# Kernel optimization log

Hardware: AMD Instinct MI355X
Metric: run time of the kernel (lower is better)

## Reference

```python
import jax, jax.numpy as jnp
import numpy as np

INV_DELTA = 15.0  # init kwarg inv_delta
EPS = 1e-12       # torch F.normalize eps


def setup_inputs() -> dict:
    key = jax.random.key(0)
    k1, k2 = jax.random.split(key)
    features = jax.random.normal(k1, (32, 256, 30, 30), dtype=jnp.float32)
    # _embedding buffer: randn clamped to >= 0
    embedding = jnp.maximum(jax.random.normal(k2, (2048, 256), dtype=jnp.float32), 0.0)
    # _min_distance_mean buffer, initialized to 0.5
    min_distance_mean = jnp.ones((1,), dtype=jnp.float32) * 0.5
    return {"features": features, "embedding": embedding,
            "min_distance_mean": min_distance_mean}


def reference(features, embedding, min_distance_mean):
    # crop 1-pixel border: [B,C,H,W] -> [B,C,H-2,W-2]
    f = features[:, :, 1:-1, 1:-1]
    # squared euclidean distance to each codeword via GEMM trick:
    # dist[b,k,h,w] = ||f[b,:,h,w]||^2 + ||e[k]||^2 - 2 <f, e[k]>
    f2 = jnp.sum(f * f, axis=1, keepdims=True)                 # [B,1,H',W']
    e2 = jnp.sum(embedding * embedding, axis=1)                # [K]
    xe = jnp.einsum('bchw,kc->bkhw', f, embedding)             # 1x1-conv GEMM
    dist = f2 + e2[None, :, None, None] - 2.0 * xe             # [B,K,H',W']
    # adaptive temperature softmax over codewords
    inv_delta_adaptive = INV_DELTA / min_distance_mean[0]
    codes = jax.nn.softmax(-inv_delta_adaptive * dist, axis=1)  # [B,K,H',W']
    # global average pool + L1 normalize
    bow = jnp.mean(codes, axis=(2, 3))                          # [B,K]
    bow = bow / jnp.maximum(jnp.sum(jnp.abs(bow), axis=1, keepdims=True), EPS)
    return (bow, codes)
```

## Files before the change

kernel.cpp:

```cpp
#include <hip/hip_runtime.h>
#include <hip/hip_bf16.h>
#include <math.h>

typedef __attribute__((ext_vector_type(8))) short bf16x8;
typedef __attribute__((ext_vector_type(16))) float f32x16;

#define B_ 32
#define C_ 256
#define K_ 2048
#define HW_ 784
#define NPIX 25088
#define FEAT_BSTRIDE 230400
#define FEAT_CSTRIDE 900
#define INV_DELTA 15.0f
#define LOG2E 1.4426950408889634f
#define QSCALE 409.6f
#define QDEC (LOG2E / QSCALE)

#define BM 128
#define BN 128
#define BKC 32
#define NCH 8
#define NSLAB 16

#define AS1 __attribute__((address_space(1)))
#define AS3 __attribute__((address_space(3)))

__device__ __forceinline__ ushort f2bf(float x) {
    __hip_bfloat16 h = __float2bfloat16(x);
    return *reinterpret_cast<ushort*>(&h);
}
__device__ __forceinline__ float bf2f(ushort u) {
    __hip_bfloat16 h;
    *reinterpret_cast<ushort*>(&h) = u;
    return __bfloat162float(h);
}
__device__ __forceinline__ void gl_lds16(const ushort* g, ushort* l) {
    __builtin_amdgcn_global_load_lds((AS1 const uint*)g, (AS3 uint*)l, 16, 0, 0);
}

__global__ void e2_kernel(const float* __restrict__ emb, float* __restrict__ e2) {
    int t = threadIdx.x;
    int wid = t >> 6, lane = t & 63;
    int k = blockIdx.x * 4 + wid;
    const float* er = emb + (size_t)k * C_;
    float v0 = er[lane], v1 = er[lane + 64], v2 = er[lane + 128], v3 = er[lane + 192];
    float s = v0 * v0 + v1 * v1 + v2 * v2 + v3 * v3;
#pragma unroll
    for (int off = 32; off > 0; off >>= 1) s += __shfl_xor(s, off);
    if (lane == 0) e2[k] = s;
}

__global__ void prep_e_kernel(const float* __restrict__ emb,
                              ushort* __restrict__ ehi, ushort* __restrict__ elo) {
    int i = blockIdx.x * 256 + threadIdx.x;
    float v = emb[i];
    ushort h = f2bf(v);
    float r = v - bf2f(h);
    ehi[i] = h;
    elo[i] = f2bf(r);
}

__global__ __launch_bounds__(256) void prep_f_kernel(const float* __restrict__ feat,
                                                     ushort* __restrict__ fhi,
                                                     ushort* __restrict__ flo) {
    __shared__ float F[256 * 65];
    int t = threadIdx.x;
    int px0 = blockIdx.x * 64;
    {
        int lane = t & 63, cq = t >> 6;
        int px = px0 + lane;
        int b = px / HW_, hw = px % HW_;
        int h = hw / 28, w = hw % 28;
        const float* base = feat + (size_t)b * FEAT_BSTRIDE + (size_t)(h + 1) * 30 + (w + 1);
#pragma unroll
        for (int cc = 0; cc < 64; ++cc) {
            int c = cq * 64 + cc;
            F[c * 65 + lane] = base[(size_t)c * FEAT_CSTRIDE];
        }
    }
    __syncthreads();
    {
        int px_l = t >> 2, cseg = t & 3;
        size_t ob = (size_t)(px0 + px_l) * C_ + cseg * 64;
        uint uh[32], ul[32];
#pragma unroll
        for (int j = 0; j < 32; ++j) {
            float v0 = F[(cseg * 64 + 2 * j) * 65 + px_l];
            float v1 = F[(cseg * 64 + 2 * j + 1) * 65 + px_l];
            ushort h0 = f2bf(v0), h1 = f2bf(v1);
            float r0 = v0 - bf2f(h0), r1 = v1 - bf2f(h1);
            uh[j] = (uint)h0 | ((uint)h1 << 16);
            ul[j] = (uint)f2bf(r0) | ((uint)f2bf(r1) << 16);
        }
#pragma unroll
        for (int j = 0; j < 8; ++j) {
            *reinterpret_cast<uint4*>(&fhi[ob + j * 8]) = *reinterpret_cast<uint4*>(&uh[j * 4]);
            *reinterpret_cast<uint4*>(&flo[ob + j * 8]) = *reinterpret_cast<uint4*>(&ul[j * 4]);
        }
    }
}

__global__ __launch_bounds__(256, 3) void gemm_kernel(
    const ushort* __restrict__ fhi, const ushort* __restrict__ flo,
    const ushort* __restrict__ ehi, const ushort* __restrict__ elo,
    const float* __restrict__ mdm, const float* __restrict__ e2g,
    ushort* __restrict__ zq, float* __restrict__ m_part, float* __restrict__ l_part)
{
    __shared__ __align__(16) ushort Asmem[2][2][BM * BKC];
    __shared__ float redA[2][132];
    __shared__ float redM[132];
    uint* zT = reinterpret_cast<uint*>(Asmem);

    int t = threadIdx.x;
    int lane = t & 63, wid = t >> 6;
    int wrow = wid >> 1, wcol = wid & 1;
    int g = lane >> 5, ci = lane & 31;

    int bid = blockIdx.x;
    int swz = (bid & 7) * 392 + (bid >> 3);
    int tile = swz >> 4, slab = swz & 15;
    int px0 = tile * BM;
    int k0 = slab * BN;

    auto stageA = [&](int buf, int ch) {
        int c0 = ch * BKC;
#pragma unroll
        for (int i = 0; i < 2; ++i) {
            int p = t + i * 256;
            int rp = p >> 3, q = p & 7;
            int v = q ^ (rp & 7);
            int row = rp * 2 + (v >> 2);
            int cu = (v & 3) * 8;
            size_t ga = (size_t)(px0 + row) * C_ + c0 + cu;
            gl_lds16(fhi + ga, &Asmem[buf][0][p * 8]);
            gl_lds16(flo + ga, &Asmem[buf][1][p * 8]);
        }
    };

    const ushort* pbh[2];
    const ushort* pbl[2];
#pragma unroll
    for (int ni = 0; ni < 2; ++ni) {
        size_t r = (size_t)(k0 + wcol * 64 + ni * 32 + ci) * C_ + g * 8;
        pbh[ni] = ehi + r;
        pbl[ni] = elo + r;
    }
    bf16x8 bhS[2][2], bvS[2][2];
    auto loadB = [&](int slot, int gs) {
        int off = gs * 16;
#pragma unroll
        for (int ni = 0; ni < 2; ++ni) {
            bhS[slot][ni] = *reinterpret_cast<const bf16x8*>(pbh[ni] + off);
            bvS[slot][ni] = *reinterpret_cast<const bf16x8*>(pbl[ni] + off);
        }
    };

    f32x16 acc[2][2];
#pragma unroll
    for (int mi = 0; mi < 2; ++mi)
#pragma unroll
        for (int ni = 0; ni < 2; ++ni)
            acc[mi][ni] = (f32x16)(0.0f);

    int xr = (ci >> 1) & 7;
    int bb4 = (ci & 1) * 4;
    int rpA0 = wrow * 32 + (ci >> 1);

    stageA(0, 0);
    loadB(0, 0);
    asm volatile("s_waitcnt vmcnt(4)" ::: "memory");
    __builtin_amdgcn_s_barrier();

#pragma unroll
    for (int ch = 0; ch < NCH; ++ch) {
        if (ch + 1 < NCH) stageA((ch + 1) & 1, ch + 1);
#pragma unroll
        for (int s = 0; s < 2; ++s) {
            int gs = ch * 2 + s;
            if (gs + 1 < 2 * NCH) loadB((gs + 1) & 1, gs + 1);
            __builtin_amdgcn_sched_barrier(0);
            int qs = (bb4 + s * 2 + g) ^ xr;
            bf16x8 ah[2], av[2];
#pragma unroll
            for (int mi = 0; mi < 2; ++mi) {
                int off = (rpA0 + mi * 16) * 64 + qs * 8;
                ah[mi] = *reinterpret_cast<const bf16x8*>(&Asmem[ch & 1][0][off]);
                av[mi] = *reinterpret_cast<const bf16x8*>(&Asmem[ch & 1][1][off]);
            }
            int cs = gs & 1;
#pragma unroll
            for (int mi = 0; mi < 2; ++mi)
#pragma unroll
                for (int ni = 0; ni < 2; ++ni) {
                    acc[mi][ni] = __builtin_amdgcn_mfma_f32_32x32x16_bf16(ah[mi], bhS[cs][ni], acc[mi][ni], 0, 0, 0);
                    acc[mi][ni] = __builtin_amdgcn_mfma_f32_32x32x16_bf16(ah[mi], bvS[cs][ni], acc[mi][ni], 0, 0, 0);
                    acc[mi][ni] = __builtin_amdgcn_mfma_f32_32x32x16_bf16(av[mi], bhS[cs][ni], acc[mi][ni], 0, 0, 0);
                }
        }
        if (ch + 1 < NCH) {
            asm volatile("s_waitcnt vmcnt(4)" ::: "memory");
            __builtin_amdgcn_s_barrier();
        }
    }

    const float alpha = INV_DELTA / mdm[0];
    float e2v[2];
#pragma unroll
    for (int ni = 0; ni < 2; ++ni) e2v[ni] = e2g[k0 + wcol * 64 + ni * 32 + ci];
#pragma unroll
    for (int mi = 0; mi < 2; ++mi)
#pragma unroll
        for (int ni = 0; ni < 2; ++ni)
            acc[mi][ni] = alpha * (2.0f * acc[mi][ni] - e2v[ni]);

    float ms[2][16];
    {
        float mt[2][16];
#pragma unroll
        for (int mi = 0; mi < 2; ++mi)
#pragma unroll
            for (int r = 0; r < 16; ++r)
                mt[mi][r] = fmaxf(acc[mi][0][r], acc[mi][1][r]);
#pragma unroll
        for (int off = 1; off < 32; off <<= 1)
#pragma unroll
            for (int mi = 0; mi < 2; ++mi)
#pragma unroll
                for (int r = 0; r < 16; ++r)
                    mt[mi][r] = fmaxf(mt[mi][r], __shfl_xor(mt[mi][r], off));
        if (ci == 0) {
#pragma unroll
            for (int mi = 0; mi < 2; ++mi)
#pragma unroll
                for (int r = 0; r < 16; ++r)
                    redA[wcol][wrow * 64 + mi * 32 + (r & 3) + 8 * (r >> 2) + 4 * g] = mt[mi][r];
        }
    }
    __syncthreads();
    if (t < 128) redM[t] = fmaxf(redA[0][t], redA[1][t]);
    __syncthreads();
#pragma unroll
    for (int mi = 0; mi < 2; ++mi)
#pragma unroll
        for (int r = 0; r < 16; ++r)
            ms[mi][r] = redM[wrow * 64 + mi * 32 + (r & 3) + 8 * (r >> 2) + 4 * g];

    {
        float lt[2][16];
#pragma unroll
        for (int mi = 0; mi < 2; ++mi)
#pragma unroll
            for (int r = 0; r < 16; ++r)
                lt[mi][r] = exp2f((acc[mi][0][r] - ms[mi][r]) * LOG2E) +
                            exp2f((acc[mi][1][r] - ms[mi][r]) * LOG2E);
#pragma unroll
        for (int off = 1; off < 32; off <<= 1)
#pragma unroll
            for (int mi = 0; mi < 2; ++mi)
#pragma unroll
                for (int r = 0; r < 16; ++r)
                    lt[mi][r] += __shfl_xor(lt[mi][r], off);
        if (ci == 0) {
#pragma unroll
            for (int mi = 0; mi < 2; ++mi)
#pragma unroll
                for (int r = 0; r < 16; ++r)
                    redA[wcol][wrow * 64 + mi * 32 + (r & 3) + 8 * (r >> 2) + 4 * g] = lt[mi][r];
        }
    }
    __syncthreads();
    if (t < 128) {
        m_part[(size_t)slab * NPIX + px0 + t] = redM[t];
        l_part[(size_t)slab * NPIX + px0 + t] = redA[0][t] + redA[1][t];
    }

#pragma unroll
    for (int mi = 0; mi < 2; ++mi)
#pragma unroll
        for (int ni = 0; ni < 2; ++ni) {
            int kl = wcol * 64 + ni * 32 + ci;
#pragma unroll
            for (int r = 0; r < 16; r += 2) {
                int row = wrow * 64 + mi * 32 + (r & 3) + 8 * (r >> 2) + 4 * g;
                float s0 = fmaxf((acc[mi][ni][r]     - ms[mi][r])     * QSCALE, -32760.f);
                float s1 = fmaxf((acc[mi][ni][r + 1] - ms[mi][r + 1]) * QSCALE, -32760.f);
                int q0 = (int)s0, q1 = (int)s1;
                uint u = ((uint)(ushort)(short)q0) | (((uint)(ushort)(short)q1) << 16);
                int pp = row >> 1;
                int seg = pp >> 2;
                zT[kl * 64 + ((seg ^ (kl & 15)) << 2) + (pp & 3)] = u;
            }
        }
    __syncthreads();

    const uint4* zT4 = reinterpret_cast<const uint4*>(zT);
#pragma unroll
    for (int it = 0; it < 8; ++it) {
        int kl = (t >> 4) + it * 16;
        int seg = t & 15;
        uint4 v = zT4[kl * 16 + (seg ^ (kl & 15))];
        int k = k0 + kl;
        int pxx = px0 + seg * 8;
        int bb = pxx / HW_, hh = pxx - bb * HW_;
        *reinterpret_cast<uint4*>(&zq[((size_t)bb * K_ + k) * HW_ + hh]) = v;
    }
}

__global__ void combine_kernel(const float* __restrict__ m_part, const float* __restrict__ l_part,
                               float* __restrict__ m_fin, float* __restrict__ rl_g) {
    int p = blockIdx.x * 256 + threadIdx.x;
    float m = -3.4e38f;
#pragma unroll
    for (int s = 0; s < NSLAB; ++s) m = fmaxf(m, m_part[(size_t)s * NPIX + p]);
    float l = 0.f;
#pragma unroll
    for (int s = 0; s < NSLAB; ++s)
        l += l_part[(size_t)s * NPIX + p] * exp2f((m_part[(size_t)s * NPIX + p] - m) * LOG2E);
    m_fin[p] = m;
    rl_g[p] = 1.0f / l;
}

__global__ __launch_bounds__(256) void finish_kernel(
    const ushort* __restrict__ zq, const float* __restrict__ m_part,
    const float* __restrict__ m_fin, const float* __restrict__ rl_g,
    float* __restrict__ codes, float* __restrict__ bow)
{
    __shared__ float corr[HW_], rls[HW_];
    __shared__ float bsum[64][4];
    int t = threadIdx.x;
    int kc = blockIdx.x, b = blockIdx.y;
    int slab = kc >> 1;
    for (int i = t; i < HW_; i += 256) {
        int p = b * HW_ + i;
        corr[i] = (m_part[(size_t)slab * NPIX + p] - m_fin[p]) * LOG2E;
        rls[i] = rl_g[p];
    }
    __syncthreads();
    int wid = t >> 6, lane = t & 63;
    for (int kl = 0; kl < 64; ++kl) {
        int k = kc * 64 + kl;
        size_t base = ((size_t)b * K_ + k) * HW_;
        float ssum = 0.f;
        if (t < 196) {
            uint2 raw = *reinterpret_cast<const uint2*>(&zq[base + t * 4]);
            int q0 = (int)(short)(raw.x & 0xffffu), q1 = (int)(short)(raw.x >> 16);
            int q2 = (int)(short)(raw.y & 0xffffu), q3 = (int)(short)(raw.y >> 16);
            float4 out;
            out.x = exp2f(fmaf((float)q0, QDEC, corr[t * 4 + 0])) * rls[t * 4 + 0];
            out.y = exp2f(fmaf((float)q1, QDEC, corr[t * 4 + 1])) * rls[t * 4 + 1];
            out.z = exp2f(fmaf((float)q2, QDEC, corr[t * 4 + 2])) * rls[t * 4 + 2];
            out.w = exp2f(fmaf((float)q3, QDEC, corr[t * 4 + 3])) * rls[t * 4 + 3];
            *reinterpret_cast<float4*>(&codes[base + t * 4]) = out;
            ssum = out.x + out.y + out.z + out.w;
        }
#pragma unroll
        for (int off = 32; off > 0; off >>= 1) ssum += __shfl_xor(ssum, off);
        if (lane == 0) bsum[kl][wid] = ssum;
    }
    __syncthreads();
    if (t < 64) {
        float s = bsum[t][0] + bsum[t][1] + bsum[t][2] + bsum[t][3];
        bow[(size_t)b * K_ + kc * 64 + t] = s * (1.0f / 784.0f);
    }
}

__global__ void bownorm_kernel(float* __restrict__ bow) {
    __shared__ float wred[4];
    __shared__ float denom_s;
    int b = blockIdx.x, t = threadIdx.x;
    float* row = bow + (size_t)b * K_;
    float v[8];
    float s = 0.f;
#pragma unroll
    for (int i = 0; i < 8; ++i) {
        v[i] = row[t + i * 256];
        s += fabsf(v[i]);
    }
#pragma unroll
    for (int off = 32; off > 0; off >>= 1) s += __shfl_xor(s, off);
    int wid = t >> 6, lane = t & 63;
    if (lane == 0) wred[wid] = s;
    __syncthreads();
    if (t == 0) denom_s = fmaxf(wred[0] + wred[1] + wred[2] + wred[3], 1e-12f);
    __syncthreads();
    float denom = denom_s;
#pragma unroll
    for (int i = 0; i < 8; ++i) row[t + i * 256] = v[i] / denom;
}

extern "C" void kernel_launch(void* const* d_in, const int* in_sizes, int n_in,
                              void* d_out, int out_size, void* d_ws, size_t ws_size,
                              hipStream_t stream) {
    const float* feat = (const float*)d_in[0];
    const float* emb  = (const float*)d_in[1];
    const float* mdm  = (const float*)d_in[2];
    float* bow   = (float*)d_out;
    float* codes = bow + (size_t)B_ * K_;

    char* ws = (char*)d_ws;
    size_t off = 0;
    auto alloc = [&](size_t bytes) { char* p = ws + off; off = (off + bytes + 255) & ~(size_t)255; return p; };
    ushort* ehi    = (ushort*)alloc((size_t)K_ * C_ * 2);
    ushort* elo    = (ushort*)alloc((size_t)K_ * C_ * 2);
    float*  e2     = (float*)alloc(K_ * 4);
    float*  m_part = (float*)alloc((size_t)NSLAB * NPIX * 4);
    float*  l_part = (float*)alloc((size_t)NSLAB * NPIX * 4);
    float*  m_fin  = (float*)alloc((size_t)NPIX * 4);
    float*  rl_g   = (float*)alloc((size_t)NPIX * 4);
    ushort* zq     = (ushort*)alloc((size_t)NPIX * K_ * 2);

    ushort* fhi = (ushort*)codes;
    ushort* flo = fhi + (size_t)NPIX * C_;

    e2_kernel<<<512, 256, 0, stream>>>(emb, e2);
    prep_e_kernel<<<2048, 256, 0, stream>>>(emb, ehi, elo);
    prep_f_kernel<<<392, 256, 0, stream>>>(feat, fhi, flo);
    gemm_kernel<<<3136, 256, 0, stream>>>(fhi, flo, ehi, elo, mdm, e2, zq, m_part, l_part);
    combine_kernel<<<98, 256, 0, stream>>>(m_part, l_part, m_fin, rl_g);
    finish_kernel<<<dim3(32, 32), 256, 0, stream>>>(zq, m_part, m_fin, rl_g, codes, bow);
    bownorm_kernel<<<32, 256, 0, stream>>>(bow);
}
```

Baseline: 233.4 us.

## Swap MFMA operands so accumulators hold per-pixel columns and store directly

The MFMA operand order is swapped so each lane's accumulator fragment covers codewords for a single pixel. The per-pixel max and sum-exp reductions then need one cross-lane shuffle instead of a five-step butterfly. The LDS transpose staging and its extra barrier before the quantized output store are removed, and each lane now writes 2-byte values straight to global memory. The risk is less efficient global writes: each row becomes a 64-byte segment of 2-byte stores instead of 16-byte vector stores, on a very large output tensor.

```diff
diff --git a/kernel.cpp b/kernel.cpp
--- a/kernel.cpp
+++ b/kernel.cpp
@@ -107,10 +107,9 @@
     const float* __restrict__ mdm, const float* __restrict__ e2g,
     ushort* __restrict__ zq, float* __restrict__ m_part, float* __restrict__ l_part)
 {
-    __shared__ __align__(16) ushort Asmem[2][2][BM * BKC];
+    __shared__ __align__(16) ushort Fsmem[2][2][BM * BKC];
     __shared__ float redA[2][132];
     __shared__ float redM[132];
-    uint* zT = reinterpret_cast<uint*>(Asmem);
 
     int t = threadIdx.x;
     int lane = t & 63, wid = t >> 6;
@@ -123,7 +122,7 @@
     int px0 = tile * BM;
     int k0 = slab * BN;
 
-    auto stageA = [&](int buf, int ch) {
+    auto stageF = [&](int buf, int ch) {
         int c0 = ch * BKC;
 #pragma unroll
         for (int i = 0; i < 2; ++i) {
@@ -133,26 +132,26 @@
             int row = rp * 2 + (v >> 2);
             int cu = (v & 3) * 8;
             size_t ga = (size_t)(px0 + row) * C_ + c0 + cu;
-            gl_lds16(fhi + ga, &Asmem[buf][0][p * 8]);
-            gl_lds16(flo + ga, &Asmem[buf][1][p * 8]);
+            gl_lds16(fhi + ga, &Fsmem[buf][0][p * 8]);
+            gl_lds16(flo + ga, &Fsmem[buf][1][p * 8]);
         }
     };
 
-    const ushort* pbh[2];
-    const ushort* pbl[2];
+    const ushort* peh[2];
+    const ushort* pel[2];
 #pragma unroll
     for (int ni = 0; ni < 2; ++ni) {
         size_t r = (size_t)(k0 + wcol * 64 + ni * 32 + ci) * C_ + g * 8;
-        pbh[ni] = ehi + r;
-        pbl[ni] = elo + r;
-    }
-    bf16x8 bhS[2][2], bvS[2][2];
-    auto loadB = [&](int slot, int gs) {
+        peh[ni] = ehi + r;
+        pel[ni] = elo + r;
+    }
+    bf16x8 ehS[2][2], elS[2][2];
+    auto loadE = [&](int slot, int gs) {
         int off = gs * 16;
 #pragma unroll
         for (int ni = 0; ni < 2; ++ni) {
-            bhS[slot][ni] = *reinterpret_cast<const bf16x8*>(pbh[ni] + off);
-            bvS[slot][ni] = *reinterpret_cast<const bf16x8*>(pbl[ni] + off);
+            ehS[slot][ni] = *reinterpret_cast<const bf16x8*>(peh[ni] + off);
+            elS[slot][ni] = *reinterpret_cast<const bf16x8*>(pel[ni] + off);
         }
     };
 
@@ -165,37 +164,37 @@
 
     int xr = (ci >> 1) & 7;
     int bb4 = (ci & 1) * 4;
-    int rpA0 = wrow * 32 + (ci >> 1);
-
-    stageA(0, 0);
-    loadB(0, 0);
-    asm volatile("s_waitcnt vmcnt(4)" ::: "memory");
+    int rpF0 = wrow * 32 + (ci >> 1);
+
+    stageF(0, 0);
+    loadE(0, 0);
+    asm volatile("s_waitcnt vmcnt(2)" ::: "memory");
     __builtin_amdgcn_s_barrier();
 
 #pragma unroll
     for (int ch = 0; ch < NCH; ++ch) {
-        if (ch + 1 < NCH) stageA((ch + 1) & 1, ch + 1);
+        if (ch + 1 < NCH) stageF((ch + 1) & 1, ch + 1);
 #pragma unroll
         for (int s = 0; s < 2; ++s) {
             int gs = ch * 2 + s;
-            if (gs + 1 < 2 * NCH) loadB((gs + 1) & 1, gs + 1);
+            if (gs + 1 < 2 * NCH) loadE((gs + 1) & 1, gs + 1);
             __builtin_amdgcn_sched_barrier(0);
             int qs = (bb4 + s * 2 + g) ^ xr;
-            bf16x8 ah[2], av[2];
+            bf16x8 fh[2], fl[2];
 #pragma unroll
             for (int mi = 0; mi < 2; ++mi) {
-                int off = (rpA0 + mi * 16) * 64 + qs * 8;
-                ah[mi] = *reinterpret_cast<const bf16x8*>(&Asmem[ch & 1][0][off]);
-                av[mi] = *reinterpret_cast<const bf16x8*>(&Asmem[ch & 1][1][off]);
+                int off = (rpF0 + mi * 16) * 64 + qs * 8;
+                fh[mi] = *reinterpret_cast<const bf16x8*>(&Fsmem[ch & 1][0][off]);
+                fl[mi] = *reinterpret_cast<const bf16x8*>(&Fsmem[ch & 1][1][off]);
             }
             int cs = gs & 1;
 #pragma unroll
             for (int mi = 0; mi < 2; ++mi)
 #pragma unroll
                 for (int ni = 0; ni < 2; ++ni) {
-                    acc[mi][ni] = __builtin_amdgcn_mfma_f32_32x32x16_bf16(ah[mi], bhS[cs][ni], acc[mi][ni], 0, 0, 0);
-                    acc[mi][ni] = __builtin_amdgcn_mfma_f32_32x32x16_bf16(ah[mi], bvS[cs][ni], acc[mi][ni], 0, 0, 0);
-                    acc[mi][ni] = __builtin_amdgcn_mfma_f32_32x32x16_bf16(av[mi], bhS[cs][ni], acc[mi][ni], 0, 0, 0);
+                    acc[mi][ni] = __builtin_amdgcn_mfma_f32_32x32x16_bf16(ehS[cs][ni], fh[mi], acc[mi][ni], 0, 0, 0);
+                    acc[mi][ni] = __builtin_amdgcn_mfma_f32_32x32x16_bf16(elS[cs][ni], fh[mi], acc[mi][ni], 0, 0, 0);
+                    acc[mi][ni] = __builtin_amdgcn_mfma_f32_32x32x16_bf16(ehS[cs][ni], fl[mi], acc[mi][ni], 0, 0, 0);
                 }
         }
         if (ch + 1 < NCH) {
@@ -205,69 +204,51 @@
     }
 
     const float alpha = INV_DELTA / mdm[0];
-    float e2v[2];
-#pragma unroll
-    for (int ni = 0; ni < 2; ++ni) e2v[ni] = e2g[k0 + wcol * 64 + ni * 32 + ci];
-#pragma unroll
-    for (int mi = 0; mi < 2; ++mi)
-#pragma unroll
-        for (int ni = 0; ni < 2; ++ni)
-            acc[mi][ni] = alpha * (2.0f * acc[mi][ni] - e2v[ni]);
-
-    float ms[2][16];
     {
-        float mt[2][16];
-#pragma unroll
-        for (int mi = 0; mi < 2; ++mi)
-#pragma unroll
-            for (int r = 0; r < 16; ++r)
-                mt[mi][r] = fmaxf(acc[mi][0][r], acc[mi][1][r]);
-#pragma unroll
-        for (int off = 1; off < 32; off <<= 1)
-#pragma unroll
-            for (int mi = 0; mi < 2; ++mi)
-#pragma unroll
-                for (int r = 0; r < 16; ++r)
-                    mt[mi][r] = fmaxf(mt[mi][r], __shfl_xor(mt[mi][r], off));
-        if (ci == 0) {
-#pragma unroll
-            for (int mi = 0; mi < 2; ++mi)
-#pragma unroll
-                for (int r = 0; r < 16; ++r)
-                    redA[wcol][wrow * 64 + mi * 32 + (r & 3) + 8 * (r >> 2) + 4 * g] = mt[mi][r];
-        }
+        const float* e2b = e2g + k0 + wcol * 64 + 4 * g;
+#pragma unroll
+        for (int ni = 0; ni < 2; ++ni)
+#pragma unroll
+            for (int q = 0; q < 4; ++q) {
+                float4 ev = *reinterpret_cast<const float4*>(e2b + ni * 32 + 8 * q);
+#pragma unroll
+                for (int mi = 0; mi < 2; ++mi) {
+                    acc[mi][ni][4 * q + 0] = alpha * (2.f * acc[mi][ni][4 * q + 0] - ev.x);
+                    acc[mi][ni][4 * q + 1] = alpha * (2.f * acc[mi][ni][4 * q + 1] - ev.y);
+                    acc[mi][ni][4 * q + 2] = alpha * (2.f * acc[mi][ni][4 * q + 2] - ev.z);
+                    acc[mi][ni][4 * q + 3] = alpha * (2.f * acc[mi][ni][4 * q + 3] - ev.w);
+                }
+            }
+    }
+
+    float mt[2];
+#pragma unroll
+    for (int mi = 0; mi < 2; ++mi) {
+        float m = acc[mi][0][0];
+#pragma unroll
+        for (int ni = 0; ni < 2; ++ni)
+#pragma unroll
+            for (int r = 0; r < 16; ++r) m = fmaxf(m, acc[mi][ni][r]);
+        m = fmaxf(m, __shfl_xor(m, 32));
+        mt[mi] = m;
+        if (lane < 32) redA[wcol][wrow * 64 + mi * 32 + ci] = m;
     }
     __syncthreads();
     if (t < 128) redM[t] = fmaxf(redA[0][t], redA[1][t]);
     __syncthreads();
-#pragma unroll
-    for (int mi = 0; mi < 2; ++mi)
-#pragma unroll
-        for (int r = 0; r < 16; ++r)
-            ms[mi][r] = redM[wrow * 64 + mi * 32 + (r & 3) + 8 * (r >> 2) + 4 * g];
-
-    {
-        float lt[2][16];
-#pragma unroll
-        for (int mi = 0; mi < 2; ++mi)
-#pragma unroll
-            for (int r = 0; r < 16; ++r)
-                lt[mi][r] = exp2f((acc[mi][0][r] - ms[mi][r]) * LOG2E) +
-                            exp2f((acc[mi][1][r] - ms[mi][r]) * LOG2E);
-#pragma unroll
-        for (int off = 1; off < 32; off <<= 1)
-#pragma unroll
-            for (int mi = 0; mi < 2; ++mi)
-#pragma unroll
-                for (int r = 0; r < 16; ++r)
-                    lt[mi][r] += __shfl_xor(lt[mi][r], off);
-        if (ci == 0) {
-#pragma unroll
-            for (int mi = 0; mi < 2; ++mi)
-#pragma unroll
-                for (int r = 0; r < 16; ++r)
-                    redA[wcol][wrow * 64 + mi * 32 + (r & 3) + 8 * (r >> 2) + 4 * g] = lt[mi][r];
-        }
+    float ms[2];
+#pragma unroll
+    for (int mi = 0; mi < 2; ++mi) ms[mi] = redM[wrow * 64 + mi * 32 + ci];
+
+#pragma unroll
+    for (int mi = 0; mi < 2; ++mi) {
+        float l = 0.f;
+#pragma unroll
+        for (int ni = 0; ni < 2; ++ni)
+#pragma unroll
+            for (int r = 0; r < 16; ++r) l += exp2f((acc[mi][ni][r] - ms[mi]) * LOG2E);
+        l += __shfl_xor(l, 32);
+        if (lane < 32) redA[wcol][wrow * 64 + mi * 32 + ci] = l;
     }
     __syncthreads();
     if (t < 128) {
@@ -276,34 +257,20 @@
     }
 
 #pragma unroll
-    for (int mi = 0; mi < 2; ++mi)
-#pragma unroll
-        for (int ni = 0; ni < 2; ++ni) {
-            int kl = wcol * 64 + ni * 32 + ci;
-#pragma unroll
-            for (int r = 0; r < 16; r += 2) {
-                int row = wrow * 64 + mi * 32 + (r & 3) + 8 * (r >> 2) + 4 * g;
-                float s0 = fmaxf((acc[mi][ni][r]     - ms[mi][r])     * QSCALE, -32760.f);
-                float s1 = fmaxf((acc[mi][ni][r + 1] - ms[mi][r + 1]) * QSCALE, -32760.f);
-                int q0 = (int)s0, q1 = (int)s1;
-                uint u = ((uint)(ushort)(short)q0) | (((uint)(ushort)(short)q1) << 16);
-                int pp = row >> 1;
-                int seg = pp >> 2;
-                zT[kl * 64 + ((seg ^ (kl & 15)) << 2) + (pp & 3)] = u;
-            }
-        }
-    __syncthreads();
-
-    const uint4* zT4 = reinterpret_cast<const uint4*>(zT);
-#pragma unroll
-    for (int it = 0; it < 8; ++it) {
-        int kl = (t >> 4) + it * 16;
-        int seg = t & 15;
-        uint4 v = zT4[kl * 16 + (seg ^ (kl & 15))];
-        int k = k0 + kl;
-        int pxx = px0 + seg * 8;
+    for (int mi = 0; mi < 2; ++mi) {
+        int pxx = px0 + wrow * 64 + mi * 32 + ci;
         int bb = pxx / HW_, hh = pxx - bb * HW_;
-        *reinterpret_cast<uint4*>(&zq[((size_t)bb * K_ + k) * HW_ + hh]) = v;
+        ushort* zb = zq + ((size_t)bb * K_ + (k0 + wcol * 64 + 4 * g)) * HW_ + hh;
+#pragma unroll
+        for (int ni = 0; ni < 2; ++ni)
+#pragma unroll
+            for (int q = 0; q < 4; ++q)
+#pragma unroll
+                for (int j = 0; j < 4; ++j) {
+                    float s0 = fmaxf((acc[mi][ni][4 * q + j] - ms[mi]) * QSCALE, -32760.f);
+                    short v = (short)(int)s0;
+                    zb[(size_t)(ni * 32 + 8 * q + j) * HW_] = (ushort)v;
+                }
     }
 }
 
```

New measurement: 229.1 us. Within noise of the previous version (-1.9%).
